# Kernel optimization log

Measured on AMD Instinct MI355X. Metric: run time of the kernel, lower is better.

Reference implementation:

```python
import jax, jax.numpy as jnp
import numpy as np

COUNTS = (15, 8, 8)  # pooling_counts; consistent with N=64


def maxpool1d(x, k, s):
    # x: [B, C, L] -> valid max pool over last dim
    return jax.lax.reduce_window(x, -jnp.inf, jax.lax.max,
                                 (1, 1, k), (1, 1, s), 'VALID')


def setup_inputs() -> dict:
    key = jax.random.key(0)
    B, C, N = 32, 512, 64
    x = jax.random.normal(key, (B, C, N), dtype=jnp.float32)
    return {"x": x}


def reference(x):
    B, C, N = x.shape
    mask2d = np.eye(N, dtype=bool)
    x2d = jnp.zeros((B, C, N, N), dtype=x.dtype)
    stride, offset = 1, 0
    for level, count in enumerate(COUNTS):
        if level != 0:
            x = maxpool1d(x, 3, 2)
        for order in range(count):
            if order != 0:
                x = maxpool1d(x, 2, 1)
            i = np.arange(0, N - offset, stride)  # static indices
            j = np.arange(offset, N, stride)
            x2d = x2d.at[:, :, i, j].set(x)
            mask2d[i, j] = True
            offset += stride
        offset += stride
        stride *= 2
    return x2d, jnp.asarray(mask2d)
```

## Files before the change

kernel.cpp:

```cpp
#include <hip/hip_runtime.h>


struct MaskTable { unsigned long long m[64]; };

constexpr MaskTable make_masks() {
    MaskTable t{};
    for (int i = 0; i < 64; ++i) {
        unsigned long long mm = 0ull;
        for (int j = i; j < 64; ++j) {
            const int d = j - i;
            const bool v = (d <= 14)
                || ((i % 2 == 0) && d >= 16 && d <= 30 && (d % 2 == 0))
                || ((i % 4 == 0) && d >= 34 && d <= 62 && (d % 4 == 2));
            if (v) mm |= (1ull << j);
        }
        t.m[i] = mm;
    }
    return t;
}

__device__ constexpr MaskTable MT = make_masks();

__global__ __launch_bounds__(256) void spmax_kernel(
    const float* __restrict__ x, float* __restrict__ out,
    float* __restrict__ mask_out, int nrow_blocks)
{
    __shared__ float4 xs4[4][16];

    const int w    = threadIdx.x >> 6;
    const int lane = threadIdx.x & 63;

    if ((int)blockIdx.x >= nrow_blocks) {
        #pragma unroll
        for (int k = 0; k < 16; ++k) {
            const int idx = (int)threadIdx.x + 256 * k;
            const int i = idx >> 6, j = idx & 63;
            const int d = j - i;
            const bool v = (d >= 0) && ((d <= 14)
                || (((i & 1) == 0) && d >= 16 && d <= 30 && ((d & 1) == 0))
                || (((i & 3) == 0) && d >= 34 && d <= 62 && ((d & 3) == 2)));
            mask_out[idx] = v ? 1.0f : 0.0f;
        }
        return;
    }

    const int row = (int)blockIdx.x * 4 + w;
    float* xsf = reinterpret_cast<float*>(&xs4[w][0]);
    xsf[lane] = x[(size_t)row * 64 + lane];
    __syncthreads();

    float* orow = out + (size_t)row * 4096;

    float r = 0.0f;
    #pragma unroll
    for (int g = 15; g >= 0; --g) {
        const float4 X = xs4[w][g];
        const float xi[4] = {X.x, X.y, X.z, X.w};
        #pragma unroll
        for (int s = 3; s >= 0; --s) {
            const int i = 4 * g + s;
            const float v = xi[s];
            const float t = fmaxf(r, v);
            r = (lane == i) ? v : t;
            const float val = ((MT.m[i] >> lane) & 1ull) ? r : 0.0f;
            orow[i * 64 + lane] = val;
        }
    }
}

extern "C" void kernel_launch(void* const* d_in, const int* in_sizes, int n_in,
                              void* d_out, int out_size, void* d_ws, size_t ws_size,
                              hipStream_t stream) {
    const float* x = (const float*)d_in[0];
    float* out = (float*)d_out;
    const int rows = in_sizes[0] / 64;
    const int nrow_blocks = rows / 4;
    float* mask_out = out + (out_size - 64 * 64);
    spmax_kernel<<<nrow_blocks + 1, 256, 0, stream>>>(x, out, mask_out, nrow_blocks);
}
```

Measured before the change: 259.2 us.

## Vectorize output stores with float4 lanes and process sixteen rows per block

Each lane now owns four consecutive output columns and keeps four running maxima, so every output row is written with float4 stores instead of scalar stores. Each block handles sixteen input rows, loaded with one float4 per thread into padded shared memory. The per-column mask is built as a 0/1 float table in shared memory and applied by multiplication instead of the constant bit-table select. The aim is fewer, wider memory transactions for a kernel dominated by output writes. The cost is building the mask table in every block, and the multiply would produce NaN if an input were infinite.

```diff
diff --git a/kernel.cpp b/kernel.cpp
--- a/kernel.cpp
+++ b/kernel.cpp
@@ -1,69 +1,77 @@
 #include <hip/hip_runtime.h>
+#include <math.h>
 
 
-struct MaskTable { unsigned long long m[64]; };
-
-constexpr MaskTable make_masks() {
-    MaskTable t{};
-    for (int i = 0; i < 64; ++i) {
-        unsigned long long mm = 0ull;
-        for (int j = i; j < 64; ++j) {
-            const int d = j - i;
-            const bool v = (d <= 14)
-                || ((i % 2 == 0) && d >= 16 && d <= 30 && (d % 2 == 0))
-                || ((i % 4 == 0) && d >= 34 && d <= 62 && (d % 4 == 2));
-            if (v) mm |= (1ull << j);
-        }
-        t.m[i] = mm;
-    }
-    return t;
+__device__ __forceinline__ bool valid_ij(int i, int j) {
+    const int d = j - i;
+    return ((unsigned)d <= 14u)
+        || (((i & 1) == 0) && (unsigned)(d - 16) <= 14u && ((d & 1) == 0))
+        || (((i & 3) == 0) && (unsigned)(d - 34) <= 28u && ((d & 3) == 2));
 }
-
-__device__ constexpr MaskTable MT = make_masks();
 
 __global__ __launch_bounds__(256) void spmax_kernel(
     const float* __restrict__ x, float* __restrict__ out,
-    float* __restrict__ mask_out, int nrow_blocks)
+    float* __restrict__ mask_out, int nblocks)
 {
-    __shared__ float4 xs4[4][16];
+    __shared__ __align__(16) float xs[16 * 68];
+    __shared__ __align__(16) float mf[64 * 64];
 
-    const int w    = threadIdx.x >> 6;
-    const int lane = threadIdx.x & 63;
+    const int tid = threadIdx.x;
 
-    if ((int)blockIdx.x >= nrow_blocks) {
+    if ((int)blockIdx.x >= nblocks) {
         #pragma unroll
         for (int k = 0; k < 16; ++k) {
-            const int idx = (int)threadIdx.x + 256 * k;
-            const int i = idx >> 6, j = idx & 63;
-            const int d = j - i;
-            const bool v = (d >= 0) && ((d <= 14)
-                || (((i & 1) == 0) && d >= 16 && d <= 30 && ((d & 1) == 0))
-                || (((i & 3) == 0) && d >= 34 && d <= 62 && ((d & 3) == 2)));
-            mask_out[idx] = v ? 1.0f : 0.0f;
+            const int idx = tid + 256 * k;
+            mask_out[idx] = valid_ij(idx >> 6, idx & 63) ? 1.0f : 0.0f;
         }
         return;
     }
 
-    const int row = (int)blockIdx.x * 4 + w;
-    float* xsf = reinterpret_cast<float*>(&xs4[w][0]);
-    xsf[lane] = x[(size_t)row * 64 + lane];
+    {
+        const float4 v = reinterpret_cast<const float4*>(x)[(size_t)blockIdx.x * 256 + tid];
+        const int r = tid >> 4, c4 = tid & 15;
+        *reinterpret_cast<float4*>(&xs[r * 68 + 4 * c4]) = v;
+    }
+    #pragma unroll
+    for (int k = 0; k < 16; ++k) {
+        const int idx = tid + 256 * k;
+        mf[idx] = valid_ij(idx >> 6, idx & 63) ? 1.0f : 0.0f;
+    }
     __syncthreads();
 
-    float* orow = out + (size_t)row * 4096;
+    const int lane = tid & 63;
+    const int w    = tid >> 6;
+    const int rg   = lane >> 4;
+    const int jq   = lane & 15;
+    const int lrow = w * 4 + rg;
+    const size_t grow = (size_t)blockIdx.x * 16 + lrow;
+    float* obase = out + grow * 4096 + 4 * jq;
+    const float* xrow = &xs[lrow * 68];
+    const float* mrow = &mf[4 * jq];
 
-    float r = 0.0f;
+    float r0 = -INFINITY, r1 = -INFINITY, r2 = -INFINITY, r3 = -INFINITY;
+
     #pragma unroll
     for (int g = 15; g >= 0; --g) {
-        const float4 X = xs4[w][g];
-        const float xi[4] = {X.x, X.y, X.z, X.w};
+        const float4 X = *reinterpret_cast<const float4*>(&xrow[4 * g]);
+        const float xi4[4] = {X.x, X.y, X.z, X.w};
         #pragma unroll
-        for (int s = 3; s >= 0; --s) {
-            const int i = 4 * g + s;
-            const float v = xi[s];
-            const float t = fmaxf(r, v);
-            r = (lane == i) ? v : t;
-            const float val = ((MT.m[i] >> lane) & 1ull) ? r : 0.0f;
-            orow[i * 64 + lane] = val;
+        for (int s3 = 3; s3 >= 0; --s3) {
+            const int i = 4 * g + s3;
+            const float v = xi4[s3];
+            r0 = fmaxf(r0, v); r1 = fmaxf(r1, v);
+            r2 = fmaxf(r2, v); r3 = fmaxf(r3, v);
+            const bool hit = (jq == (i >> 2));
+            switch (i & 3) {
+                case 0: r0 = hit ? v : r0; break;
+                case 1: r1 = hit ? v : r1; break;
+                case 2: r2 = hit ? v : r2; break;
+                case 3: r3 = hit ? v : r3; break;
+            }
+            const float4 m = *reinterpret_cast<const float4*>(&mrow[i * 64]);
+            float4 o;
+            o.x = r0 * m.x; o.y = r1 * m.y; o.z = r2 * m.z; o.w = r3 * m.w;
+            *reinterpret_cast<float4*>(obase + i * 64) = o;
         }
     }
 }
@@ -74,7 +82,7 @@
     const float* x = (const float*)d_in[0];
     float* out = (float*)d_out;
     const int rows = in_sizes[0] / 64;
-    const int nrow_blocks = rows / 4;
+    const int nblocks = rows / 16;
     float* mask_out = out + (out_size - 64 * 64);
-    spmax_kernel<<<nrow_blocks + 1, 256, 0, stream>>>(x, out, mask_out, nrow_blocks);
+    spmax_kernel<<<nblocks + 1, 256, 0, stream>>>(x, out, mask_out, nblocks);
 }
```

Result: faster. 253.6 us (-2.2%).
